# Performance work log

Measured on AMD Instinct MI355X. Metric: run time of the kernel, lower is better.

Reference implementation:

```python
import jax, jax.numpy as jnp
import numpy as np

TEMP = 0.01            # entropy temperature
THRESH = 0.92          # hamming similarity threshold
BETA = 0.25            # commitment weight
ENT_W = 0.1            # entropy loss weight


def _l2_normalize(x, axis=-1, eps=1e-12):
    n = jnp.sqrt(jnp.sum(x * x, axis=axis, keepdims=True))
    return x / jnp.maximum(n, eps)


def _entropy_loss(affinity):
    # affinity: [N, K] codebook affinities (cosine similarities)
    fa = affinity / TEMP
    probs = jax.nn.softmax(fa, axis=-1)
    log_probs = jax.nn.log_softmax(fa + 1e-5, axis=-1)
    avg_probs = jnp.mean(probs, axis=0)
    avg_entropy = -jnp.sum(avg_probs * jnp.log(avg_probs + 1e-5))
    sample_entropy = -jnp.mean(jnp.sum(probs * log_probs, axis=-1))
    return sample_entropy - avg_entropy


def _hamming_consistency_loss(input_blocks, z_e):
    # binary occupancy: non-air voxels -> 1
    binary = (jnp.argmax(input_blocks, axis=1) != 0).astype(jnp.float32)  # [B,24,24,24]
    B = binary.shape[0]
    # faithful to torch: plain reshapes (no transpose)
    patterns = binary.reshape(B, 6, 4, 6, 4, 6, 4).reshape(B, 6, 6, 6, 64).reshape(-1, 64)
    N = patterns.shape[0]
    P = patterns
    # pairwise hamming distance via two Gram matmuls
    ham = P @ (1.0 - P).T + (1.0 - P) @ P.T          # [N,N]
    sim = 1.0 - ham / 64.0
    mask = (sim > THRESH) & (~jnp.eye(N, dtype=bool))
    W = jax.lax.stop_gradient(jnp.where(mask, sim, 0.0))  # detached weights
    # pre-quant embeddings per chunk, l2-normalized; cosine distance matrix
    emb = jnp.transpose(z_e, (0, 2, 3, 4, 1)).reshape(N, -1)  # [N, C]
    en = _l2_normalize(emb, axis=1)
    cos = en @ en.T                                   # [N,N]
    dist = 1.0 - cos
    return jnp.sum(dist * W) / (jnp.sum(W) + 1e-8)


def setup_inputs() -> dict:
    key = jax.random.key(0)
    k1, k2, k3 = jax.random.split(key, 3)
    input_blocks = jax.random.normal(k1, (16, 32, 24, 24, 24), dtype=jnp.float32)
    z_e = jax.random.normal(k2, (16, 256, 6, 6, 6), dtype=jnp.float32)
    codebook = jax.random.normal(k3, (1024, 256), dtype=jnp.float32)
    return {"input_blocks": input_blocks, "z_e": z_e, "codebook": codebook}


def reference(input_blocks, z_e, codebook):
    B, C, H, W, D = z_e.shape
    z = jnp.transpose(z_e, (0, 2, 3, 4, 1)).reshape(-1, C)   # [N, C]
    zn = _l2_normalize(z, axis=1)
    en = _l2_normalize(codebook, axis=1)                      # [K, C]
    affinity = zn @ en.T                                      # [N, K]
    idx = jnp.argmax(affinity, axis=1)                        # max cosine == min L2 on sphere
    z_q = en[idx]                                             # [N, C]
    sg = jax.lax.stop_gradient
    codebook_loss = jnp.mean((z_q - sg(zn)) ** 2)
    commit_loss = BETA * jnp.mean((sg(z_q) - zn) ** 2)
    ent_loss = ENT_W * _entropy_loss(affinity)
    ham_loss = _hamming_consistency_loss(input_blocks, z_e)
    loss = codebook_loss + commit_loss + ent_loss + ham_loss
    # straight-through estimator
    z_q_ste = zn + sg(z_q - zn)
    z_q_out = jnp.transpose(z_q_ste.reshape(B, H, W, D, C), (0, 4, 1, 2, 3))
    return z_q_out, loss, idx
```

## Files before the change

### kernel.cpp

```cpp
#include <hip/hip_runtime.h>
#include <cstdint>
#include <cstddef>

#define N_ROWS 3456
#define C_DIM 256
#define K_CB 1024
#define B_SZ 16
#define SPATIAL 216
#define VOX 13824
#define NCH 32
#define NSB 54

typedef __attribute__((ext_vector_type(16))) float f32x16;
typedef __attribute__((ext_vector_type(8))) short bf16x8;

__device__ __forceinline__ unsigned short f2bf_rne(float f) {
    unsigned int u = __float_as_uint(f);
    u += 0x7FFFu + ((u >> 16) & 1u);
    return (unsigned short)(u >> 16);
}
__device__ __forceinline__ float bf2f(unsigned short h) {
    unsigned int u = ((unsigned int)h) << 16;
    return __uint_as_float(u);
}

__global__ __launch_bounds__(256) void k_pre(
        const float* __restrict__ in, const float* __restrict__ cb,
        const float* __restrict__ ze,
        unsigned long long* __restrict__ pats,
        float* __restrict__ scal,
        float* __restrict__ en,
        unsigned short* __restrict__ ehi, unsigned short* __restrict__ elo,
        unsigned short* __restrict__ zhi, unsigned short* __restrict__ zlo) {
    int bid = blockIdx.x;
    int t = threadIdx.x;
    if (bid < 864) {
        if (bid == 0 && t < 16) scal[t] = 0.0f;
        int v = bid * 256 + t;
        int b = v / VOX;
        int r = v % VOX;
        const float* p = in + (size_t)b * NCH * VOX + r;
        float v0 = p[0];
        float mx = -INFINITY;
#pragma unroll
        for (int c = 1; c < NCH; ++c) mx = fmaxf(mx, p[(size_t)c * VOX]);
        unsigned long long m = __ballot(mx > v0);
        if ((t & 63) == 0) pats[v >> 6] = m;
        return;
    }
    __shared__ float ws[4];
    if (bid < 1888) {
        int k = bid - 864, c = t;
        float v = cb[k * C_DIM + c];
        float ss = v * v;
#pragma unroll
        for (int off = 32; off > 0; off >>= 1) ss += __shfl_down(ss, off, 64);
        if ((c & 63) == 0) ws[c >> 6] = ss;
        __syncthreads();
        float nrm = fmaxf(sqrtf(ws[0] + ws[1] + ws[2] + ws[3]), 1e-12f);
        float o = v / nrm;
        en[k * C_DIM + c] = o;
        unsigned short h = f2bf_rne(o);
        ehi[k * C_DIM + c] = h;
        elo[k * C_DIM + c] = f2bf_rne(o - bf2f(h));
    } else {
        int n = bid - 1888, c = t;
        int b = n / SPATIAL, s = n % SPATIAL;
        float v = ze[((size_t)(b * C_DIM + c)) * SPATIAL + s];
        float ss = v * v;
#pragma unroll
        for (int off = 32; off > 0; off >>= 1) ss += __shfl_down(ss, off, 64);
        if ((c & 63) == 0) ws[c >> 6] = ss;
        __syncthreads();
        float nrm = fmaxf(sqrtf(ws[0] + ws[1] + ws[2] + ws[3]), 1e-12f);
        float o = v / nrm;
        unsigned short h = f2bf_rne(o);
        zhi[n * C_DIM + c] = h;
        zlo[n * C_DIM + c] = f2bf_rne(o - bf2f(h));
    }
}

#define GS 72
#define HSTR 72
__global__ __launch_bounds__(128) void k_mid(
        const unsigned short* __restrict__ zhi, const unsigned short* __restrict__ zlo,
        const unsigned short* __restrict__ ehi, const unsigned short* __restrict__ elo,
        const unsigned long long* __restrict__ pats,
        float* __restrict__ aff, float* __restrict__ scal) {
    __shared__ __align__(16) char smem[55296];
    int t = threadIdx.x;
    int w = t >> 6, lane = t & 63;
    int bid = blockIdx.x;

    if (bid < 432) {
        unsigned short* Ah = (unsigned short*)smem;
        unsigned short* Al = Ah + 64 * GS;
        unsigned short* Bh = (unsigned short*)(smem + 18432);
        unsigned short* Bl = Bh + 128 * GS;
        int i0 = (bid % 54) * 64, j0 = (bid / 54) * 128;

        f32x16 acc[2][2];
#pragma unroll
        for (int r = 0; r < 2; ++r)
#pragma unroll
            for (int q = 0; q < 2; ++q)
#pragma unroll
                for (int e = 0; e < 16; ++e) acc[r][q][e] = 0.0f;

        for (int ck = 0; ck < 4; ++ck) {
            __syncthreads();
#pragma unroll
            for (int l = 0; l < 4; ++l) {
                int s = l * 128 + t;
                int row = s >> 3, c8 = s & 7;
                *(float4*)&Ah[row * GS + c8 * 8] =
                    *(const float4*)&zhi[(size_t)(i0 + row) * C_DIM + ck * 64 + c8 * 8];
                *(float4*)&Al[row * GS + c8 * 8] =
                    *(const float4*)&zlo[(size_t)(i0 + row) * C_DIM + ck * 64 + c8 * 8];
            }
#pragma unroll
            for (int l = 0; l < 8; ++l) {
                int s = l * 128 + t;
                int row = s >> 3, c8 = s & 7;
                *(float4*)&Bh[row * GS + c8 * 8] =
                    *(const float4*)&ehi[(size_t)(j0 + row) * C_DIM + ck * 64 + c8 * 8];
                *(float4*)&Bl[row * GS + c8 * 8] =
                    *(const float4*)&elo[(size_t)(j0 + row) * C_DIM + ck * 64 + c8 * 8];
            }
            __syncthreads();

#pragma unroll
            for (int ks = 0; ks < 4; ++ks) {
                int koff = (lane >> 5) * 8 + ks * 16;
                bf16x8 ah[2], al[2], bh[2], bl[2];
#pragma unroll
                for (int r = 0; r < 2; ++r) {
                    ah[r] = *(bf16x8*)&Ah[(r * 32 + (lane & 31)) * GS + koff];
                    al[r] = *(bf16x8*)&Al[(r * 32 + (lane & 31)) * GS + koff];
                }
#pragma unroll
                for (int q = 0; q < 2; ++q) {
                    bh[q] = *(bf16x8*)&Bh[(w * 64 + q * 32 + (lane & 31)) * GS + koff];
                    bl[q] = *(bf16x8*)&Bl[(w * 64 + q * 32 + (lane & 31)) * GS + koff];
                }
#pragma unroll
                for (int r = 0; r < 2; ++r)
#pragma unroll
                    for (int q = 0; q < 2; ++q) {
                        acc[r][q] = __builtin_amdgcn_mfma_f32_32x32x16_bf16(ah[r], bh[q], acc[r][q], 0, 0, 0);
                        acc[r][q] = __builtin_amdgcn_mfma_f32_32x32x16_bf16(ah[r], bl[q], acc[r][q], 0, 0, 0);
                        acc[r][q] = __builtin_amdgcn_mfma_f32_32x32x16_bf16(al[r], bh[q], acc[r][q], 0, 0, 0);
                    }
            }
        }
#pragma unroll
        for (int r = 0; r < 2; ++r)
#pragma unroll
            for (int q = 0; q < 2; ++q)
#pragma unroll
                for (int g = 0; g < 16; ++g) {
                    int row = i0 + r * 32 + (g & 3) + 8 * (g >> 2) + 4 * (lane >> 5);
                    int col = j0 + w * 64 + q * 32 + (lane & 31);
                    aff[(size_t)row * K_CB + col] = acc[r][q][g];
                }
        return;
    }

    unsigned short* zi = (unsigned short*)smem;
    unsigned short* zj = zi + 128 * HSTR;
    int hb = bid - 432;
    int ti = 0, rem = hb;
    while (rem >= 27 - ti) { rem -= 27 - ti; ++ti; }
    int tj = ti + rem;
    int i0 = ti * 128, j0 = tj * 128;
    float factor = (ti == tj) ? 1.0f : 2.0f;

    f32x16 acc[2][4];
#pragma unroll
    for (int a = 0; a < 2; ++a)
#pragma unroll
        for (int b = 0; b < 4; ++b)
#pragma unroll
            for (int e = 0; e < 16; ++e) acc[a][b][e] = 0.0f;

    for (int ck = 0; ck < 4; ++ck) {
        __syncthreads();
#pragma unroll
        for (int p = 0; p < 8; ++p) {
            int row = p * 16 + (t >> 3);
            int seg = t & 7;
            *(float4*)&zi[row * HSTR + seg * 8] =
                *(const float4*)&zhi[(size_t)(i0 + row) * C_DIM + ck * 64 + seg * 8];
            *(float4*)&zj[row * HSTR + seg * 8] =
                *(const float4*)&zhi[(size_t)(j0 + row) * C_DIM + ck * 64 + seg * 8];
        }
        __syncthreads();

#pragma unroll
        for (int ks = 0; ks < 4; ++ks) {
            int off = (lane & 31) * HSTR + (lane >> 5) * 8 + ks * 16;
            bf16x8 a0 = *(bf16x8*)&zi[(w * 64) * HSTR + off];
            bf16x8 a1 = *(bf16x8*)&zi[(w * 64 + 32) * HSTR + off];
            bf16x8 bf[4];
#pragma unroll
            for (int c = 0; c < 4; ++c)
                bf[c] = *(bf16x8*)&zj[(c * 32) * HSTR + off];
#pragma unroll
            for (int c = 0; c < 4; ++c) {
                acc[0][c] = __builtin_amdgcn_mfma_f32_32x32x16_bf16(a0, bf[c], acc[0][c], 0, 0, 0);
                acc[1][c] = __builtin_amdgcn_mfma_f32_32x32x16_bf16(a1, bf[c], acc[1][c], 0, 0, 0);
            }
        }
    }

    unsigned long long pj[4];
#pragma unroll
    for (int c = 0; c < 4; ++c) pj[c] = pats[j0 + c * 32 + (lane & 31)];

    float sW = 0.0f, sD = 0.0f;
#pragma unroll
    for (int r = 0; r < 2; ++r) {
        int ibase = i0 + w * 64 + r * 32 + 4 * (lane >> 5);
#pragma unroll
        for (int g = 0; g < 16; ++g) {
            int gi = ibase + (g & 3) + 8 * (g >> 2);
            unsigned long long pi = pats[gi];
#pragma unroll
            for (int c = 0; c < 4; ++c) {
                int gj = j0 + c * 32 + (lane & 31);
                int pop = __popcll(pi ^ pj[c]);
                float wgt = (pop <= 5 && gi != gj) ? (1.0f - (float)pop * 0.015625f) : 0.0f;
                sW += wgt;
                sD += wgt * acc[r][c][g];
            }
        }
    }
#pragma unroll
    for (int off = 32; off > 0; off >>= 1) {
        sW += __shfl_down(sW, off, 64);
        sD += __shfl_down(sD, off, 64);
    }
    if (lane == 0) {
        atomicAdd(&scal[2], factor * sW);
        atomicAdd(&scal[3], factor * sD);
    }
}

#define ZQS 257
__global__ __launch_bounds__(256) void k_post(
        const float* __restrict__ aff, const float* __restrict__ en,
        float* __restrict__ avgp_part, float* __restrict__ scal,
        float* __restrict__ out) {
    __shared__ float lps[4][K_CB];
    __shared__ float zq[64 * ZQS];
    __shared__ float lsc[8];
    __shared__ float ws4[4];
    __shared__ int lastflag;
    unsigned int* done = (unsigned int*)&scal[8];
    int t = threadIdx.x;
    int lane = t & 63, w = t >> 6;
    int n0 = blockIdx.x * 64 + w * 16;

    float ps[16];
#pragma unroll
    for (int i = 0; i < 16; ++i) ps[i] = 0.0f;
    float se = 0.0f, cm = 0.0f;

    for (int r = 0; r < 16; ++r) {
        int row = n0 + r;
        const float* ap = aff + (size_t)row * K_CB;
        float4 v[4];
#pragma unroll
        for (int j = 0; j < 4; ++j)
            v[j] = *(const float4*)&ap[j * 256 + lane * 4];

        float m = v[0].x; int mi = lane * 4;
#pragma unroll
        for (int j = 0; j < 4; ++j)
#pragma unroll
            for (int i = 0; i < 4; ++i) {
                float x = ((const float*)&v[j])[i];
                int col = j * 256 + lane * 4 + i;
                if (x > m) { m = x; mi = col; }
            }
#pragma unroll
        for (int off = 32; off > 0; off >>= 1) {
            float vo = __shfl_down(m, off, 64);
            int   io = __shfl_down(mi, off, 64);
            if (vo > m || (vo == m && io < mi)) { m = vo; mi = io; }
        }
        m = __shfl(m, 0, 64);
        mi = __shfl(mi, 0, 64);

        float e[16];
        float S = 0.0f, T = 0.0f;
#pragma unroll
        for (int j = 0; j < 4; ++j)
#pragma unroll
            for (int i = 0; i < 4; ++i) {
                float d = 100.0f * (((const float*)&v[j])[i] - m);
                float ee = __expf(d);
                e[j * 4 + i] = ee; S += ee; T += ee * d;
            }
#pragma unroll
        for (int off = 32; off > 0; off >>= 1) {
            S += __shfl_down(S, off, 64);
            T += __shfl_down(T, off, 64);
        }
        S = __shfl(S, 0, 64);
        T = __shfl(T, 0, 64);
        float invS = 1.0f / S;
#pragma unroll
        for (int i = 0; i < 16; ++i) ps[i] += e[i] * invS;
        se += logf(S) - T * invS;
        cm += 2.0f - 2.0f * m;
        if (lane == 0) out[884737 + row] = (float)mi;

        float4 g4 = *(const float4*)&en[(size_t)mi * C_DIM + lane * 4];
        int lr = w * 16 + r;
        zq[lr * ZQS + lane * 4 + 0] = g4.x;
        zq[lr * ZQS + lane * 4 + 1] = g4.y;
        zq[lr * ZQS + lane * 4 + 2] = g4.z;
        zq[lr * ZQS + lane * 4 + 3] = g4.w;
    }

#pragma unroll
    for (int j = 0; j < 4; ++j)
#pragma unroll
        for (int i = 0; i < 4; ++i)
            lps[w][j * 256 + lane * 4 + i] = ps[j * 4 + i];
    if (lane == 0) { lsc[w] = se; lsc[4 + w] = cm; }
    __syncthreads();
#pragma unroll
    for (int c = 0; c < 4; ++c) {
        int col = t * 4 + c;
        avgp_part[(size_t)blockIdx.x * K_CB + col] =
            lps[0][col] + lps[1][col] + lps[2][col] + lps[3][col];
    }
    if (t == 0) atomicAdd(&scal[0], lsc[0] + lsc[1] + lsc[2] + lsc[3]);
    if (t == 1) atomicAdd(&scal[1], lsc[4] + lsc[5] + lsc[6] + lsc[7]);

    {
        int n = blockIdx.x * 64 + lane;
        int b = n / SPATIAL, s = n - b * SPATIAL;
        size_t obase = ((size_t)b * C_DIM) * SPATIAL + s;
        for (int cc = 0; cc < 64; ++cc) {
            int c = cc * 4 + w;
            out[obase + (size_t)c * SPATIAL] = zq[lane * ZQS + c];
        }
    }

    __syncthreads();
    if (t == 0) {
        __threadfence();
        unsigned int old = atomicAdd(done, 1u);
        lastflag = (old == NSB - 1) ? 1 : 0;
    }
    __syncthreads();
    if (lastflag) {
        __threadfence();
        float term = 0.0f;
#pragma unroll
        for (int j = 0; j < 4; ++j) {
            int col = t + 256 * j;
            float ap = 0.0f;
            for (int bb = 0; bb < NSB; ++bb)
                ap += avgp_part[(size_t)bb * K_CB + col];
            ap *= (1.0f / N_ROWS);
            term += ap * logf(ap + 1e-5f);
        }
#pragma unroll
        for (int off = 32; off > 0; off >>= 1) term += __shfl_down(term, off, 64);
        if ((t & 63) == 0) ws4[t >> 6] = term;
        __syncthreads();
        if (t == 0) {
            float sAP = ws4[0] + ws4[1] + ws4[2] + ws4[3];
            float s0 = atomicAdd(&scal[0], 0.0f);
            float s1 = atomicAdd(&scal[1], 0.0f);
            float s2 = atomicAdd(&scal[2], 0.0f);
            float s3 = atomicAdd(&scal[3], 0.0f);
            float sample = s0 * (1.0f / N_ROWS);
            float commit = s1 * (1.0f / ((float)N_ROWS * C_DIM));
            float ent = 0.1f * (sample + sAP);
            float ham = (s2 - s3) / (s2 + 1e-8f);
            out[884736] = 1.25f * commit + ent + ham;
        }
    }
}

extern "C" void kernel_launch(void* const* d_in, const int* in_sizes, int n_in,
                              void* d_out, int out_size, void* d_ws, size_t ws_size,
                              hipStream_t stream) {
    const float* in_blocks = (const float*)d_in[0];
    const float* z_e       = (const float*)d_in[1];
    const float* cb        = (const float*)d_in[2];
    float* out = (float*)d_out;

    char* ws = (char*)d_ws;
    float* en   = (float*)(ws + 0);
    float* aff  = (float*)(ws + 1048576);
    unsigned short* zhi = (unsigned short*)(ws + 15204352);
    unsigned short* zlo = (unsigned short*)(ws + 16973824);
    unsigned short* ehi = (unsigned short*)(ws + 18743296);
    unsigned short* elo = (unsigned short*)(ws + 19267584);
    unsigned long long* pats = (unsigned long long*)(ws + 19791872);
    float* avgp_part = (float*)(ws + 19819520);
    float* scal = (float*)(ws + 20040704);

    k_pre<<<5344, 256, 0, stream>>>(in_blocks, cb, z_e, pats, scal,
                                    en, ehi, elo, zhi, zlo);
    k_mid<<<810, 128, 0, stream>>>(zhi, zlo, ehi, elo, pats, aff, scal);
    k_post<<<NSB, 256, 0, stream>>>(aff, en, avgp_part, scal, out);
}
```

Measured before the change: 159.5 us.

## Store bf16 operands in MFMA-fragment swizzled layout and load directly from global

```diff
diff --git a/kernel.cpp b/kernel.cpp
--- a/kernel.cpp
+++ b/kernel.cpp
@@ -22,6 +22,10 @@
 __device__ __forceinline__ float bf2f(unsigned short h) {
     unsigned int u = ((unsigned int)h) << 16;
     return __uint_as_float(u);
+}
+
+__device__ __forceinline__ size_t swz(int n, int c) {
+    return (size_t)(n >> 5) * 8192 + (size_t)((c >> 3) * 256) + (size_t)((n & 31) * 8) + (c & 7);
 }
 
 __global__ __launch_bounds__(256) void k_pre(
@@ -61,8 +65,9 @@
         float o = v / nrm;
         en[k * C_DIM + c] = o;
         unsigned short h = f2bf_rne(o);
-        ehi[k * C_DIM + c] = h;
-        elo[k * C_DIM + c] = f2bf_rne(o - bf2f(h));
+        size_t off = swz(k, c);
+        ehi[off] = h;
+        elo[off] = f2bf_rne(o - bf2f(h));
     } else {
         int n = bid - 1888, c = t;
         int b = n / SPATIAL, s = n % SPATIAL;
@@ -75,29 +80,30 @@
         float nrm = fmaxf(sqrtf(ws[0] + ws[1] + ws[2] + ws[3]), 1e-12f);
         float o = v / nrm;
         unsigned short h = f2bf_rne(o);
-        zhi[n * C_DIM + c] = h;
-        zlo[n * C_DIM + c] = f2bf_rne(o - bf2f(h));
-    }
-}
-
-#define GS 72
-#define HSTR 72
+        size_t off = swz(n, c);
+        zhi[off] = h;
+        zlo[off] = f2bf_rne(o - bf2f(h));
+    }
+}
+
 __global__ __launch_bounds__(128) void k_mid(
         const unsigned short* __restrict__ zhi, const unsigned short* __restrict__ zlo,
         const unsigned short* __restrict__ ehi, const unsigned short* __restrict__ elo,
         const unsigned long long* __restrict__ pats,
         float* __restrict__ aff, float* __restrict__ scal) {
-    __shared__ __align__(16) char smem[55296];
     int t = threadIdx.x;
     int w = t >> 6, lane = t & 63;
     int bid = blockIdx.x;
+    const bf16x8* __restrict__ Zh = (const bf16x8*)zhi;
+    const bf16x8* __restrict__ Zl = (const bf16x8*)zlo;
+    const bf16x8* __restrict__ Eh = (const bf16x8*)ehi;
+    const bf16x8* __restrict__ El = (const bf16x8*)elo;
 
     if (bid < 432) {
-        unsigned short* Ah = (unsigned short*)smem;
-        unsigned short* Al = Ah + 64 * GS;
-        unsigned short* Bh = (unsigned short*)(smem + 18432);
-        unsigned short* Bl = Bh + 128 * GS;
-        int i0 = (bid % 54) * 64, j0 = (bid / 54) * 128;
+        int ib = bid % 54, jb = bid / 54;
+        int i0 = ib * 64, j0 = jb * 128;
+        int sa = ib * 2;
+        int sb = jb * 4 + w * 2;
 
         f32x16 acc[2][2];
 #pragma unroll
@@ -107,51 +113,28 @@
 #pragma unroll
                 for (int e = 0; e < 16; ++e) acc[r][q][e] = 0.0f;
 
-        for (int ck = 0; ck < 4; ++ck) {
-            __syncthreads();
-#pragma unroll
-            for (int l = 0; l < 4; ++l) {
-                int s = l * 128 + t;
-                int row = s >> 3, c8 = s & 7;
-                *(float4*)&Ah[row * GS + c8 * 8] =
-                    *(const float4*)&zhi[(size_t)(i0 + row) * C_DIM + ck * 64 + c8 * 8];
-                *(float4*)&Al[row * GS + c8 * 8] =
-                    *(const float4*)&zlo[(size_t)(i0 + row) * C_DIM + ck * 64 + c8 * 8];
-            }
-#pragma unroll
-            for (int l = 0; l < 8; ++l) {
-                int s = l * 128 + t;
-                int row = s >> 3, c8 = s & 7;
-                *(float4*)&Bh[row * GS + c8 * 8] =
-                    *(const float4*)&ehi[(size_t)(j0 + row) * C_DIM + ck * 64 + c8 * 8];
-                *(float4*)&Bl[row * GS + c8 * 8] =
-                    *(const float4*)&elo[(size_t)(j0 + row) * C_DIM + ck * 64 + c8 * 8];
-            }
-            __syncthreads();
-
-#pragma unroll
-            for (int ks = 0; ks < 4; ++ks) {
-                int koff = (lane >> 5) * 8 + ks * 16;
-                bf16x8 ah[2], al[2], bh[2], bl[2];
-#pragma unroll
-                for (int r = 0; r < 2; ++r) {
-                    ah[r] = *(bf16x8*)&Ah[(r * 32 + (lane & 31)) * GS + koff];
-                    al[r] = *(bf16x8*)&Al[(r * 32 + (lane & 31)) * GS + koff];
+#pragma unroll
+        for (int s16 = 0; s16 < 16; ++s16) {
+            int u = s16 * 64 + lane;
+            bf16x8 ah[2], al[2], bh[2], bl[2];
+#pragma unroll
+            for (int r = 0; r < 2; ++r) {
+                ah[r] = Zh[(size_t)(sa + r) * 1024 + u];
+                al[r] = Zl[(size_t)(sa + r) * 1024 + u];
+            }
+#pragma unroll
+            for (int q = 0; q < 2; ++q) {
+                bh[q] = Eh[(size_t)(sb + q) * 1024 + u];
+                bl[q] = El[(size_t)(sb + q) * 1024 + u];
+            }
+#pragma unroll
+            for (int r = 0; r < 2; ++r)
+#pragma unroll
+                for (int q = 0; q < 2; ++q) {
+                    acc[r][q] = __builtin_amdgcn_mfma_f32_32x32x16_bf16(ah[r], bh[q], acc[r][q], 0, 0, 0);
+                    acc[r][q] = __builtin_amdgcn_mfma_f32_32x32x16_bf16(ah[r], bl[q], acc[r][q], 0, 0, 0);
+                    acc[r][q] = __builtin_amdgcn_mfma_f32_32x32x16_bf16(al[r], bh[q], acc[r][q], 0, 0, 0);
                 }
-#pragma unroll
-                for (int q = 0; q < 2; ++q) {
-                    bh[q] = *(bf16x8*)&Bh[(w * 64 + q * 32 + (lane & 31)) * GS + koff];
-                    bl[q] = *(bf16x8*)&Bl[(w * 64 + q * 32 + (lane & 31)) * GS + koff];
-                }
-#pragma unroll
-                for (int r = 0; r < 2; ++r)
-#pragma unroll
-                    for (int q = 0; q < 2; ++q) {
-                        acc[r][q] = __builtin_amdgcn_mfma_f32_32x32x16_bf16(ah[r], bh[q], acc[r][q], 0, 0, 0);
-                        acc[r][q] = __builtin_amdgcn_mfma_f32_32x32x16_bf16(ah[r], bl[q], acc[r][q], 0, 0, 0);
-                        acc[r][q] = __builtin_amdgcn_mfma_f32_32x32x16_bf16(al[r], bh[q], acc[r][q], 0, 0, 0);
-                    }
-            }
         }
 #pragma unroll
         for (int r = 0; r < 2; ++r)
@@ -166,14 +149,14 @@
         return;
     }
 
-    unsigned short* zi = (unsigned short*)smem;
-    unsigned short* zj = zi + 128 * HSTR;
     int hb = bid - 432;
     int ti = 0, rem = hb;
     while (rem >= 27 - ti) { rem -= 27 - ti; ++ti; }
     int tj = ti + rem;
     int i0 = ti * 128, j0 = tj * 128;
     float factor = (ti == tj) ? 1.0f : 2.0f;
+    int si = ti * 4 + w * 2;
+    int sj = tj * 4;
 
     f32x16 acc[2][4];
 #pragma unroll
@@ -183,33 +166,19 @@
 #pragma unroll
             for (int e = 0; e < 16; ++e) acc[a][b][e] = 0.0f;
 
-    for (int ck = 0; ck < 4; ++ck) {
-        __syncthreads();
-#pragma unroll
-        for (int p = 0; p < 8; ++p) {
-            int row = p * 16 + (t >> 3);
-            int seg = t & 7;
-            *(float4*)&zi[row * HSTR + seg * 8] =
-                *(const float4*)&zhi[(size_t)(i0 + row) * C_DIM + ck * 64 + seg * 8];
-            *(float4*)&zj[row * HSTR + seg * 8] =
-                *(const float4*)&zhi[(size_t)(j0 + row) * C_DIM + ck * 64 + seg * 8];
-        }
-        __syncthreads();
-
-#pragma unroll
-        for (int ks = 0; ks < 4; ++ks) {
-            int off = (lane & 31) * HSTR + (lane >> 5) * 8 + ks * 16;
-            bf16x8 a0 = *(bf16x8*)&zi[(w * 64) * HSTR + off];
-            bf16x8 a1 = *(bf16x8*)&zi[(w * 64 + 32) * HSTR + off];
-            bf16x8 bf[4];
-#pragma unroll
-            for (int c = 0; c < 4; ++c)
-                bf[c] = *(bf16x8*)&zj[(c * 32) * HSTR + off];
-#pragma unroll
-            for (int c = 0; c < 4; ++c) {
-                acc[0][c] = __builtin_amdgcn_mfma_f32_32x32x16_bf16(a0, bf[c], acc[0][c], 0, 0, 0);
-                acc[1][c] = __builtin_amdgcn_mfma_f32_32x32x16_bf16(a1, bf[c], acc[1][c], 0, 0, 0);
-            }
+#pragma unroll
+    for (int s16 = 0; s16 < 16; ++s16) {
+        int u = s16 * 64 + lane;
+        bf16x8 a0 = Zh[(size_t)si * 1024 + u];
+        bf16x8 a1 = Zh[(size_t)(si + 1) * 1024 + u];
+        bf16x8 bf[4];
+#pragma unroll
+        for (int c = 0; c < 4; ++c)
+            bf[c] = Zh[(size_t)(sj + c) * 1024 + u];
+#pragma unroll
+        for (int c = 0; c < 4; ++c) {
+            acc[0][c] = __builtin_amdgcn_mfma_f32_32x32x16_bf16(a0, bf[c], acc[0][c], 0, 0, 0);
+            acc[1][c] = __builtin_amdgcn_mfma_f32_32x32x16_bf16(a1, bf[c], acc[1][c], 0, 0, 0);
         }
     }
 
```

Result: no change. 159.5 us (+0.0%).
